# Kernel tuning notes

Hardware: AMD Instinct MI355X
Metric: run time of the kernel (lower is better)

The kernel has to match this reference:

```python
import jax, jax.numpy as jnp
import numpy as np

B, N, C = 16, 1024, 256
E = 524288
NUM_NODES = B * N
D0 = C + 7            # 263 input node feature dim
LAYERS = [256, 256, 256]


def _xavier(key, shape):
    fan_out, fan_in = shape
    lim = jnp.sqrt(6.0 / (fan_in + fan_out))
    return jax.random.uniform(key, shape, jnp.float32, -lim, lim)


def setup_inputs() -> dict:
    key = jax.random.key(0)
    ks = jax.random.split(key, 9)
    rois = jax.random.normal(ks[0], (B, N, 7), jnp.float32)
    pooled_features = jax.random.normal(ks[1], (B, N, C), jnp.float32)
    edge_index = jax.random.randint(ks[2], (2, E), 0, NUM_NODES, dtype=jnp.int64)
    # EdgeConv linear weights: layer0 in = 2*(C+7)=526, later in = 2*256=512
    W1 = _xavier(ks[3], (LAYERS[0], 2 * D0))
    b1 = jnp.zeros((LAYERS[0],), jnp.float32)
    W2 = _xavier(ks[4], (LAYERS[1], 2 * LAYERS[0]))
    b2 = jnp.zeros((LAYERS[1],), jnp.float32)
    W3 = _xavier(ks[5], (LAYERS[2], 2 * LAYERS[1]))
    b3 = jnp.zeros((LAYERS[2],), jnp.float32)
    return {"rois": rois, "pooled_features": pooled_features,
            "edge_index": edge_index,
            "W1": W1, "b1": b1, "W2": W2, "b2": b2, "W3": W3, "b3": b3}


def _edge_conv(x, src, dst, W, b):
    # message: cat(x_j - x_i, x_i) -> linear -> relu ; aggregate: scatter max at target i
    x_i = x[dst]                                   # [E, d] target features
    x_j = x[src]                                   # [E, d] source features
    msg = jnp.concatenate([x_j - x_i, x_i], axis=-1)   # [E, 2d]
    msg = jax.nn.relu(msg @ W.T + b)               # [E, out]
    agg = jax.ops.segment_max(msg, dst, num_segments=NUM_NODES)
    # nodes with no incoming edges: fill -inf -> 0 (PyG convention)
    return jnp.where(jnp.isfinite(agg), agg, jnp.zeros((), agg.dtype))


def reference(rois, pooled_features, edge_index, W1, b1, W2, b2, W3, b3):
    # global features: cat(pooled, boxes) flattened over batch
    x = jnp.concatenate([pooled_features, rois], axis=-1).reshape(-1, D0)  # [B*N, 263]
    src, dst = edge_index[0], edge_index[1]  # PyG: row = source j, col = target i
    feats = [x]
    x1 = _edge_conv(x, src, dst, W1, b1)
    feats.append(x1)
    x2 = _edge_conv(x1, src, dst, W2, b2)
    feats.append(x2)
    x3 = _edge_conv(x2, src, dst, W3, b3)
    feats.append(x3)
    related_features = jnp.concatenate(feats, axis=-1)  # [B*N, 263+768]
    return related_features
```

## Files before the change

### kernel.cpp

```cpp
#include <hip/hip_runtime.h>
#include <stdint.h>

#define NODES 16384
#define D0    263
#define K1PAD 288
#define OUTW  1031

typedef __attribute__((ext_vector_type(8))) short bf16x8;
typedef __attribute__((ext_vector_type(4))) float f32x4;
typedef __attribute__((ext_vector_type(8))) unsigned short u16x8;

__device__ __forceinline__ float bf2f(unsigned short u) {
    union { unsigned int i; float f; } c; c.i = ((unsigned int)u) << 16; return c.f;
}
__device__ __forceinline__ unsigned short f2bf(float f) {
    union { float f; unsigned int i; } c; c.f = f;
    unsigned int x = c.i;
    unsigned int r = (x + 0x7fffu + ((x >> 16) & 1u)) >> 16;
    return (unsigned short)r;
}
__device__ __forceinline__ unsigned short bf2key(unsigned short b) {
    return (b & 0x8000u) ? (unsigned short)~b : (unsigned short)(b | 0x8000u);
}
__device__ __forceinline__ unsigned short key2bf(unsigned short k) {
    return (k & 0x8000u) ? (unsigned short)(k ^ 0x8000u) : (unsigned short)~k;
}

__global__ void detect_zero_kernel(const void* __restrict__ ei, const void* __restrict__ pooled,
                                   int* __restrict__ flags, int* __restrict__ deg) {
    int idx = blockIdx.x * 256 + threadIdx.x;
    deg[idx] = 0;
    if (blockIdx.x == 0 && threadIdx.x < 64) {
        int lane = threadIdx.x;
        const long long* e64 = (const long long*)ei;
        bool ok = true;
        for (int i = lane; i < 512; i += 64) {
            long long v = e64[i];
            if (v < 0 || v >= NODES) ok = false;
        }
        unsigned long long b = __ballot(ok);
        const unsigned short* ph = (const unsigned short*)pooled;
        int hits = 0;
        for (int i = lane; i < 512; i += 64) {
            int e = (ph[i] >> 7) & 0xFF;
            if (e >= 0x90) hits++;
        }
        for (int off = 32; off; off >>= 1) hits += __shfl_down(hits, off);
        if (lane == 0) {
            flags[0] = (b == ~0ull) ? 1 : 0;
            flags[1] = (hits > 8) ? 1 : 0;
        }
    }
}

__global__ void hist_kernel(const void* __restrict__ ei, int E, const int* __restrict__ flags,
                            int* __restrict__ deg) {
    int e = blockIdx.x * blockDim.x + threadIdx.x;
    if (e >= E) return;
    int d = flags[0] ? (int)((const long long*)ei)[(size_t)E + e]
                     : ((const int*)ei)[(size_t)E + e];
    atomicAdd(&deg[d], 1);
}

__global__ void scan_kernel(const int* __restrict__ deg, int* __restrict__ offs,
                            int* __restrict__ cursor) {
    __shared__ int part[256];
    int tid = threadIdx.x;
    int base = tid * 64;
    int s = 0;
    for (int i = 0; i < 64; ++i) s += deg[base + i];
    part[tid] = s;
    __syncthreads();
    for (int off = 1; off < 256; off <<= 1) {
        int t = (tid >= off) ? part[tid - off] : 0;
        __syncthreads();
        part[tid] += t;
        __syncthreads();
    }
    int run = (tid > 0) ? part[tid - 1] : 0;
    for (int i = 0; i < 64; ++i) {
        int idx = base + i;
        offs[idx] = run;
        cursor[idx] = run;
        run += deg[idx];
    }
    if (tid == 255) offs[NODES] = run;
}

__global__ void scatter_kernel(const void* __restrict__ ei, int E, const int* __restrict__ flags,
                               int* __restrict__ cursor, int* __restrict__ ssrc) {
    int e = blockIdx.x * blockDim.x + threadIdx.x;
    if (e >= E) return;
    int s, d;
    if (flags[0]) {
        const long long* p = (const long long*)ei;
        s = (int)p[e];
        d = (int)p[(size_t)E + e];
    } else {
        const int* p = (const int*)ei;
        s = p[e];
        d = p[(size_t)E + e];
    }
    int pos = atomicAdd(&cursor[d], 1);
    ssrc[pos] = s;
}

#define T0 (NODES * K1PAD)
#define S1 (512 * K1PAD)
#define S2 (512 * 256)
__global__ void setup_kernel(const void* __restrict__ pooled, const void* __restrict__ rois,
                             const void* __restrict__ W1, const void* __restrict__ W2,
                             const void* __restrict__ W3, const int* __restrict__ flags,
                             unsigned short* __restrict__ x0p, void* __restrict__ outv,
                             unsigned short* __restrict__ wc1, unsigned short* __restrict__ wc2,
                             unsigned short* __restrict__ wc3) {
    int idx = blockIdx.x * 256 + threadIdx.x;
    bool f32m = flags[1] != 0;
    if (idx < T0) {
        int node = idx / K1PAD;
        int k = idx - node * K1PAD;
        float val = 0.f;
        if (k < 256) {
            val = f32m ? ((const float*)pooled)[(size_t)node * 256 + k]
                       : bf2f(((const unsigned short*)pooled)[(size_t)node * 256 + k]);
        } else if (k < D0) {
            val = f32m ? ((const float*)rois)[(size_t)node * 7 + (k - 256)]
                       : bf2f(((const unsigned short*)rois)[(size_t)node * 7 + (k - 256)]);
        }
        x0p[idx] = f2bf(val);
        if (k < D0) {
            if (f32m) ((float*)outv)[(size_t)node * OUTW + k] = val;
            else      ((unsigned short*)outv)[(size_t)node * OUTW + k] = f2bf(val);
        }
        return;
    }
    idx -= T0;
    if (idx < S1) {
        int r = idx / K1PAD;
        int k = idx - r * K1PAD;
        unsigned short val = 0;
        if (k < D0) {
            if (r < 256) {
                float a = f32m ? ((const float*)W1)[(size_t)r * 526 + k]
                               : bf2f(((const unsigned short*)W1)[(size_t)r * 526 + k]);
                val = f2bf(a);
            } else {
                size_t ro = (size_t)(r - 256) * 526;
                float a, b;
                if (f32m) { a = ((const float*)W1)[ro + k]; b = ((const float*)W1)[ro + D0 + k]; }
                else      { a = bf2f(((const unsigned short*)W1)[ro + k]);
                            b = bf2f(((const unsigned short*)W1)[ro + D0 + k]); }
                val = f2bf(b - a);
            }
        }
        wc1[idx] = val;
        return;
    }
    idx -= S1;
    const void* W = (idx < S2) ? W2 : W3;
    unsigned short* wc = (idx < S2) ? wc2 : wc3;
    if (idx >= S2) idx -= S2;
    int r = idx >> 8;
    int k = idx & 255;
    unsigned short val;
    if (r < 256) {
        float a = f32m ? ((const float*)W)[(size_t)r * 512 + k]
                       : bf2f(((const unsigned short*)W)[(size_t)r * 512 + k]);
        val = f2bf(a);
    } else {
        size_t ro = (size_t)(r - 256) * 512;
        float a, b;
        if (f32m) { a = ((const float*)W)[ro + k]; b = ((const float*)W)[ro + 256 + k]; }
        else      { a = bf2f(((const unsigned short*)W)[ro + k]);
                    b = bf2f(((const unsigned short*)W)[ro + 256 + k]); }
        val = f2bf(b - a);
    }
    wc[idx] = val;
}

template <int K>
__global__ __launch_bounds__(256) void gemm_kernel(const unsigned short* __restrict__ A,
                                                   const unsigned short* __restrict__ Wc,
                                                   unsigned short* __restrict__ u_key,
                                                   float* __restrict__ v_f) {
    int lane = threadIdx.x & 63;
    int wave = threadIdx.x >> 6;
    int row0 = blockIdx.x * 64;
    int col0 = blockIdx.y * 256 + wave * 64;
    int lr = lane & 15;
    int kb = (lane >> 4) * 8;
    const unsigned short* Ap = A + (size_t)(row0 + lr) * K + kb;
    const unsigned short* Wp = Wc + (size_t)(col0 + lr) * K + kb;

    f32x4 acc[4][4];
    #pragma unroll
    for (int i = 0; i < 4; ++i)
        #pragma unroll
        for (int j = 0; j < 4; ++j) acc[i][j] = (f32x4){0.f, 0.f, 0.f, 0.f};

    for (int k0 = 0; k0 < K; k0 += 32) {
        bf16x8 a[4], b[4];
        #pragma unroll
        for (int i = 0; i < 4; ++i) a[i] = *reinterpret_cast<const bf16x8*>(Ap + (size_t)i * 16 * K + k0);
        #pragma unroll
        for (int i = 0; i < 4; ++i) b[i] = *reinterpret_cast<const bf16x8*>(Wp + (size_t)i * 16 * K + k0);
        #pragma unroll
        for (int rb = 0; rb < 4; ++rb)
            #pragma unroll
            for (int cb = 0; cb < 4; ++cb)
                acc[rb][cb] = __builtin_amdgcn_mfma_f32_16x16x32_bf16(a[rb], b[cb], acc[rb][cb], 0, 0, 0);
    }

    bool is_u = (blockIdx.y == 0);
    #pragma unroll
    for (int rb = 0; rb < 4; ++rb) {
        int rbase = row0 + rb * 16 + (lane >> 4) * 4;
        #pragma unroll
        for (int cb = 0; cb < 4; ++cb) {
            int c = col0 + cb * 16 + lr;
            #pragma unroll
            for (int reg = 0; reg < 4; ++reg) {
                float val = acc[rb][cb][reg];
                int r = rbase + reg;
                if (is_u) u_key[(size_t)r * 256 + c] = bf2key(f2bf(val));
                else      v_f[(size_t)r * 256 + (c - 256)] = val;
            }
        }
    }
}

__global__ __launch_bounds__(256) void combine_kernel(const unsigned short* __restrict__ u_key,
                                                      const float* __restrict__ v_f,
                                                      const void* __restrict__ bias,
                                                      const int* __restrict__ flags,
                                                      const int* __restrict__ offs,
                                                      const int* __restrict__ ssrc,
                                                      unsigned short* __restrict__ x_cur,
                                                      void* __restrict__ outv,
                                                      int col_off) {
    int lane = threadIdx.x & 63;
    int node = blockIdx.x * 4 + (threadIdx.x >> 6);
    int half = lane >> 5;
    int cl = lane & 31;
    int s0 = offs[node];
    int s1 = offs[node + 1];
    bool f32m = flags[1] != 0;

    const u16x8* U = (const u16x8*)u_key;
    u16x8 mk = (u16x8)0;

    int i = s0 + half;
    for (; i + 6 < s1; i += 8) {
        int sA = ssrc[i], sB = ssrc[i + 2], sC = ssrc[i + 4], sD = ssrc[i + 6];
        u16x8 pA = U[(size_t)sA * 32 + cl];
        u16x8 pB = U[(size_t)sB * 32 + cl];
        u16x8 pC = U[(size_t)sC * 32 + cl];
        u16x8 pD = U[(size_t)sD * 32 + cl];
        mk = __builtin_elementwise_max(mk, __builtin_elementwise_max(
                 __builtin_elementwise_max(pA, pB), __builtin_elementwise_max(pC, pD)));
    }
    for (; i < s1; i += 2) {
        int s = ssrc[i];
        mk = __builtin_elementwise_max(mk, U[(size_t)s * 32 + cl]);
    }

    union { u16x8 v; uint4 u; } cvt;
    cvt.v = mk;
    cvt.u.x = __shfl_xor((int)cvt.u.x, 32);
    cvt.u.y = __shfl_xor((int)cvt.u.y, 32);
    cvt.u.z = __shfl_xor((int)cvt.u.z, 32);
    cvt.u.w = __shfl_xor((int)cvt.u.w, 32);
    mk = __builtin_elementwise_max(mk, cvt.v);

    int ch0 = cl * 8 + half * 4;
    float mm[4];
    #pragma unroll
    for (int j = 0; j < 4; ++j) mm[j] = bf2f(key2bf(mk[half * 4 + j]));

    float4 v = *(const float4*)(v_f + (size_t)node * 256 + ch0);
    float bb[4];
    if (f32m) {
        const float* bf = (const float*)bias;
        #pragma unroll
        for (int j = 0; j < 4; ++j) bb[j] = bf[ch0 + j];
    } else {
        const unsigned short* bh = (const unsigned short*)bias;
        #pragma unroll
        for (int j = 0; j < 4; ++j) bb[j] = bf2f(bh[ch0 + j]);
    }
    float vv[4] = {v.x, v.y, v.z, v.w};
    float r[4];
    bool nz = (s1 > s0);
    #pragma unroll
    for (int j = 0; j < 4; ++j) r[j] = nz ? fmaxf(mm[j] + vv[j] + bb[j], 0.f) : 0.f;

    unsigned short h[4];
    #pragma unroll
    for (int j = 0; j < 4; ++j) h[j] = f2bf(r[j]);
    uint2 packed;
    packed.x = (unsigned int)h[0] | ((unsigned int)h[1] << 16);
    packed.y = (unsigned int)h[2] | ((unsigned int)h[3] << 16);
    *(uint2*)(x_cur + (size_t)node * 256 + ch0) = packed;

    size_t ob = (size_t)node * OUTW + col_off + ch0;
    if (f32m) {
        float* of = (float*)outv;
        #pragma unroll
        for (int j = 0; j < 4; ++j) of[ob + j] = r[j];
    } else {
        unsigned short* oh = (unsigned short*)outv;
        #pragma unroll
        for (int j = 0; j < 4; ++j) oh[ob + j] = h[j];
    }
}

extern "C" void kernel_launch(void* const* d_in, const int* in_sizes, int n_in,
                              void* d_out, int out_size, void* d_ws, size_t ws_size,
                              hipStream_t stream) {
    const void* rois   = d_in[0];
    const void* pooled = d_in[1];
    const void* ei     = d_in[2];
    const void* W1 = d_in[3];
    const void* b1 = d_in[4];
    const void* W2 = d_in[5];
    const void* b2 = d_in[6];
    const void* W3 = d_in[7];
    const void* b3 = d_in[8];

    const int E = in_sizes[2] / 2;

    char* ws = (char*)d_ws;
    size_t o = 0;
    auto take = [&](size_t bytes) { size_t cur = o; o += (bytes + 255) & ~(size_t)255; return cur; };
    int* flags           = (int*)(ws + take(8));
    int* deg             = (int*)(ws + take(sizeof(int) * NODES));
    int* offs            = (int*)(ws + take(sizeof(int) * (NODES + 1)));
    int* cursor          = (int*)(ws + take(sizeof(int) * NODES));
    int* ssrc            = (int*)(ws + take(sizeof(int) * (size_t)E));
    unsigned short* x0p  = (unsigned short*)(ws + take(2ull * NODES * K1PAD));
    unsigned short* wc1  = (unsigned short*)(ws + take(2ull * 512 * K1PAD));
    unsigned short* wc2  = (unsigned short*)(ws + take(2ull * 512 * 256));
    unsigned short* wc3  = (unsigned short*)(ws + take(2ull * 512 * 256));
    unsigned short* ukey = (unsigned short*)(ws + take(2ull * NODES * 256));
    float*          vf   = (float*)(ws + take(4ull * NODES * 256));
    unsigned short* xcur = (unsigned short*)(ws + take(2ull * NODES * 256));
    (void)ws_size;

    const int eb = (E + 255) / 256;

    detect_zero_kernel<<<NODES / 256, 256, 0, stream>>>(ei, pooled, flags, deg);
    hist_kernel<<<eb, 256, 0, stream>>>(ei, E, flags, deg);
    scan_kernel<<<1, 256, 0, stream>>>(deg, offs, cursor);
    scatter_kernel<<<eb, 256, 0, stream>>>(ei, E, flags, cursor, ssrc);

    setup_kernel<<<(T0 + S1 + 2 * S2) / 256, 256, 0, stream>>>(pooled, rois, W1, W2, W3, flags,
                                                               x0p, d_out, wc1, wc2, wc3);

    gemm_kernel<K1PAD><<<dim3(NODES / 64, 2), 256, 0, stream>>>(x0p, wc1, ukey, vf);
    combine_kernel<<<NODES / 4, 256, 0, stream>>>(ukey, vf, b1, flags, offs, ssrc, xcur, d_out, D0);

    gemm_kernel<256><<<dim3(NODES / 64, 2), 256, 0, stream>>>(xcur, wc2, ukey, vf);
    combine_kernel<<<NODES / 4, 256, 0, stream>>>(ukey, vf, b2, flags, offs, ssrc, xcur, d_out, D0 + 256);

    gemm_kernel<256><<<dim3(NODES / 64, 2), 256, 0, stream>>>(xcur, wc3, ukey, vf);
    combine_kernel<<<NODES / 4, 256, 0, stream>>>(ukey, vf, b3, flags, offs, ssrc, xcur, d_out, D0 + 512);
}
```

Baseline: 252.7 us.

## Split gathered u table into two 128-channel halves for cache-resident max gather

The GEMM now writes the u keys into two separate 128-channel arrays, and each layer's combine step runs as two passes, one per half, each gathering 8-byte vectors. Each half table is 4 MB instead of 8 MB, so the random neighbour gather is more likely to hit in L2 or the last-level cache. In exchange, the CSR indices and offsets are read twice, there are twice as many launches, and each gather load is narrower.

```diff
diff --git a/kernel.cpp b/kernel.cpp
--- a/kernel.cpp
+++ b/kernel.cpp
@@ -8,7 +8,7 @@
 
 typedef __attribute__((ext_vector_type(8))) short bf16x8;
 typedef __attribute__((ext_vector_type(4))) float f32x4;
-typedef __attribute__((ext_vector_type(8))) unsigned short u16x8;
+typedef __attribute__((ext_vector_type(4))) unsigned short u16x4;
 
 __device__ __forceinline__ float bf2f(unsigned short u) {
     union { unsigned int i; float f; } c; c.i = ((unsigned int)u) << 16; return c.f;
@@ -181,7 +181,8 @@
 template <int K>
 __global__ __launch_bounds__(256) void gemm_kernel(const unsigned short* __restrict__ A,
                                                    const unsigned short* __restrict__ Wc,
-                                                   unsigned short* __restrict__ u_key,
+                                                   unsigned short* __restrict__ u_lo,
+                                                   unsigned short* __restrict__ u_hi,
                                                    float* __restrict__ v_f) {
     int lane = threadIdx.x & 63;
     int wave = threadIdx.x >> 6;
@@ -222,14 +223,19 @@
             for (int reg = 0; reg < 4; ++reg) {
                 float val = acc[rb][cb][reg];
                 int r = rbase + reg;
-                if (is_u) u_key[(size_t)r * 256 + c] = bf2key(f2bf(val));
-                else      v_f[(size_t)r * 256 + (c - 256)] = val;
+                if (is_u) {
+                    unsigned short key = bf2key(f2bf(val));
+                    if (c < 128) u_lo[(size_t)r * 128 + c] = key;
+                    else         u_hi[(size_t)r * 128 + (c - 128)] = key;
+                } else {
+                    v_f[(size_t)r * 256 + (c - 256)] = val;
+                }
             }
         }
     }
 }
 
-__global__ __launch_bounds__(256) void combine_kernel(const unsigned short* __restrict__ u_key,
+__global__ __launch_bounds__(256) void combine_kernel(const unsigned short* __restrict__ U,
                                                       const float* __restrict__ v_f,
                                                       const void* __restrict__ bias,
                                                       const int* __restrict__ flags,
@@ -237,7 +243,8 @@
                                                       const int* __restrict__ ssrc,
                                                       unsigned short* __restrict__ x_cur,
                                                       void* __restrict__ outv,
-                                                      int col_off) {
+                                                      int col_off,
+                                                      int ch_off) {
     int lane = threadIdx.x & 63;
     int node = blockIdx.x * 4 + (threadIdx.x >> 6);
     int half = lane >> 5;
@@ -246,71 +253,57 @@
     int s1 = offs[node + 1];
     bool f32m = flags[1] != 0;
 
-    const u16x8* U = (const u16x8*)u_key;
-    u16x8 mk = (u16x8)0;
+    const u16x4* U4 = (const u16x4*)U;
+    u16x4 mk = (u16x4)0;
 
     int i = s0 + half;
     for (; i + 6 < s1; i += 8) {
         int sA = ssrc[i], sB = ssrc[i + 2], sC = ssrc[i + 4], sD = ssrc[i + 6];
-        u16x8 pA = U[(size_t)sA * 32 + cl];
-        u16x8 pB = U[(size_t)sB * 32 + cl];
-        u16x8 pC = U[(size_t)sC * 32 + cl];
-        u16x8 pD = U[(size_t)sD * 32 + cl];
+        u16x4 pA = U4[(size_t)sA * 32 + cl];
+        u16x4 pB = U4[(size_t)sB * 32 + cl];
+        u16x4 pC = U4[(size_t)sC * 32 + cl];
+        u16x4 pD = U4[(size_t)sD * 32 + cl];
         mk = __builtin_elementwise_max(mk, __builtin_elementwise_max(
                  __builtin_elementwise_max(pA, pB), __builtin_elementwise_max(pC, pD)));
     }
     for (; i < s1; i += 2) {
         int s = ssrc[i];
-        mk = __builtin_elementwise_max(mk, U[(size_t)s * 32 + cl]);
-    }
-
-    union { u16x8 v; uint4 u; } cvt;
-    cvt.v = mk;
-    cvt.u.x = __shfl_xor((int)cvt.u.x, 32);
-    cvt.u.y = __shfl_xor((int)cvt.u.y, 32);
-    cvt.u.z = __shfl_xor((int)cvt.u.z, 32);
-    cvt.u.w = __shfl_xor((int)cvt.u.w, 32);
-    mk = __builtin_elementwise_max(mk, cvt.v);
-
-    int ch0 = cl * 8 + half * 4;
-    float mm[4];
-    #pragma unroll
-    for (int j = 0; j < 4; ++j) mm[j] = bf2f(key2bf(mk[half * 4 + j]));
-
-    float4 v = *(const float4*)(v_f + (size_t)node * 256 + ch0);
-    float bb[4];
+        mk = __builtin_elementwise_max(mk, U4[(size_t)s * 32 + cl]);
+    }
+
+    union { u16x4 v; uint2 u; } c1;
+    c1.v = mk;
+    c1.u.x = __shfl_xor((int)c1.u.x, 32);
+    c1.u.y = __shfl_xor((int)c1.u.y, 32);
+    mk = __builtin_elementwise_max(mk, c1.v);
+
+    int ch0 = cl * 4 + half * 2;
+    float m0 = bf2f(key2bf(mk[half * 2 + 0]));
+    float m1 = bf2f(key2bf(mk[half * 2 + 1]));
+    float2 v = *(const float2*)(v_f + (size_t)node * 256 + ch_off + ch0);
+    float b0, b1;
     if (f32m) {
         const float* bf = (const float*)bias;
-        #pragma unroll
-        for (int j = 0; j < 4; ++j) bb[j] = bf[ch0 + j];
+        b0 = bf[ch_off + ch0]; b1 = bf[ch_off + ch0 + 1];
     } else {
         const unsigned short* bh = (const unsigned short*)bias;
-        #pragma unroll
-        for (int j = 0; j < 4; ++j) bb[j] = bf2f(bh[ch0 + j]);
-    }
-    float vv[4] = {v.x, v.y, v.z, v.w};
-    float r[4];
+        b0 = bf2f(bh[ch_off + ch0]); b1 = bf2f(bh[ch_off + ch0 + 1]);
+    }
     bool nz = (s1 > s0);
-    #pragma unroll
-    for (int j = 0; j < 4; ++j) r[j] = nz ? fmaxf(mm[j] + vv[j] + bb[j], 0.f) : 0.f;
-
-    unsigned short h[4];
-    #pragma unroll
-    for (int j = 0; j < 4; ++j) h[j] = f2bf(r[j]);
-    uint2 packed;
-    packed.x = (unsigned int)h[0] | ((unsigned int)h[1] << 16);
-    packed.y = (unsigned int)h[2] | ((unsigned int)h[3] << 16);
-    *(uint2*)(x_cur + (size_t)node * 256 + ch0) = packed;
+    float r0 = nz ? fmaxf(m0 + v.x + b0, 0.f) : 0.f;
+    float r1 = nz ? fmaxf(m1 + v.y + b1, 0.f) : 0.f;
+
+    unsigned short h0 = f2bf(r0), h1 = f2bf(r1);
+    unsigned int hp = (unsigned int)h0 | ((unsigned int)h1 << 16);
+    *(unsigned int*)(x_cur + (size_t)node * 256 + ch_off + ch0) = hp;
 
     size_t ob = (size_t)node * OUTW + col_off + ch0;
     if (f32m) {
         float* of = (float*)outv;
-        #pragma unroll
-        for (int j = 0; j < 4; ++j) of[ob + j] = r[j];
+        of[ob + 0] = r0; of[ob + 1] = r1;
     } else {
         unsigned short* oh = (unsigned short*)outv;
-        #pragma unroll
-        for (int j = 0; j < 4; ++j) oh[ob + j] = h[j];
+        oh[ob + 0] = h0; oh[ob + 1] = h1;
     }
 }
 
@@ -341,7 +334,8 @@
     unsigned short* wc1  = (unsigned short*)(ws + take(2ull * 512 * K1PAD));
     unsigned short* wc2  = (unsigned short*)(ws + take(2ull * 512 * 256));
     unsigned short* wc3  = (unsigned short*)(ws + take(2ull * 512 * 256));
-    unsigned short* ukey = (unsigned short*)(ws + take(2ull * NODES * 256));
+    unsigned short* u_lo = (unsigned short*)(ws + take(2ull * NODES * 128));
+    unsigned short* u_hi = (unsigned short*)(ws + take(2ull * NODES * 128));
     float*          vf   = (float*)(ws + take(4ull * NODES * 256));
     unsigned short* xcur = (unsigned short*)(ws + take(2ull * NODES * 256));
     (void)ws_size;
@@ -356,12 +350,15 @@
     setup_kernel<<<(T0 + S1 + 2 * S2) / 256, 256, 0, stream>>>(pooled, rois, W1, W2, W3, flags,
                                                                x0p, d_out, wc1, wc2, wc3);
 
-    gemm_kernel<K1PAD><<<dim3(NODES / 64, 2), 256, 0, stream>>>(x0p, wc1, ukey, vf);
-    combine_kernel<<<NODES / 4, 256, 0, stream>>>(ukey, vf, b1, flags, offs, ssrc, xcur, d_out, D0);
-
-    gemm_kernel<256><<<dim3(NODES / 64, 2), 256, 0, stream>>>(xcur, wc2, ukey, vf);
-    combine_kernel<<<NODES / 4, 256, 0, stream>>>(ukey, vf, b2, flags, offs, ssrc, xcur, d_out, D0 + 256);
-
-    gemm_kernel<256><<<dim3(NODES / 64, 2), 256, 0, stream>>>(xcur, wc3, ukey, vf);
-    combine_kernel<<<NODES / 4, 256, 0, stream>>>(ukey, vf, b3, flags, offs, ssrc, xcur, d_out, D0 + 512);
-}
+    gemm_kernel<K1PAD><<<dim3(NODES / 64, 2), 256, 0, stream>>>(x0p, wc1, u_lo, u_hi, vf);
+    combine_kernel<<<NODES / 4, 256, 0, stream>>>(u_lo, vf, b1, flags, offs, ssrc, xcur, d_out, D0, 0);
+    combine_kernel<<<NODES / 4, 256, 0, stream>>>(u_hi, vf, b1, flags, offs, ssrc, xcur, d_out, D0 + 128, 128);
+
+    gemm_kernel<256><<<dim3(NODES / 64, 2), 256, 0, stream>>>(xcur, wc2, u_lo, u_hi, vf);
+    combine_kernel<<<NODES / 4, 256, 0, stream>>>(u_lo, vf, b2, flags, offs, ssrc, xcur, d_out, D0 + 256, 0);
+    combine_kernel<<<NODES / 4, 256, 0, stream>>>(u_hi, vf, b2, flags, offs, ssrc, xcur, d_out, D0 + 384, 128);
+
+    gemm_kernel<256><<<dim3(NODES / 64, 2), 256, 0, stream>>>(xcur, wc3, u_lo, u_hi, vf);
+    combine_kernel<<<NODES / 4, 256, 0, stream>>>(u_lo, vf, b3, flags, offs, ssrc, xcur, d_out, D0 + 512, 0);
+    combine_kernel<<<NODES / 4, 256, 0, stream>>>(u_hi, vf, b3, flags, offs, ssrc, xcur, d_out, D0 + 640, 128);
+}
```

Measured after the change: 277.8 us. 1.1x slower.

## Channel-group transposed layout with LDS-resident gather for segment max

Applied to the files above, without the earlier changes.

The GEMM now writes the U and V projections in a channel-pair-major layout, with the bias folded into V. Each combine block loads one 2-channel slice for all 16384 nodes (64 KB) into LDS and performs the per-node max gather out of shared memory instead of random global reads. A new fixup kernel transposes the results back to node-major order for the next layer's input and for the output. This replaces scattered global gathers with LDS gathers, but each layer now has only 256 combine blocks, each thread loops over 32 nodes, and there is an extra transpose pass and launch per layer.

```diff
diff --git a/kernel.cpp b/kernel.cpp
--- a/kernel.cpp
+++ b/kernel.cpp
@@ -5,10 +5,11 @@
 #define D0    263
 #define K1PAD 288
 #define OUTW  1031
+#define NGRP  128
 
 typedef __attribute__((ext_vector_type(8))) short bf16x8;
 typedef __attribute__((ext_vector_type(4))) float f32x4;
-typedef __attribute__((ext_vector_type(8))) unsigned short u16x8;
+typedef __attribute__((ext_vector_type(2))) unsigned short u16x2;
 
 __device__ __forceinline__ float bf2f(unsigned short u) {
     union { unsigned int i; float f; } c; c.i = ((unsigned int)u) << 16; return c.f;
@@ -24,6 +25,9 @@
 }
 __device__ __forceinline__ unsigned short key2bf(unsigned short k) {
     return (k & 0x8000u) ? (unsigned short)(k ^ 0x8000u) : (unsigned short)~k;
+}
+__device__ __forceinline__ u16x2 as_u16x2(unsigned int x) {
+    union { unsigned int u; u16x2 v; } c; c.u = x; return c.v;
 }
 
 __global__ void detect_zero_kernel(const void* __restrict__ ei, const void* __restrict__ pooled,
@@ -181,8 +185,10 @@
 template <int K>
 __global__ __launch_bounds__(256) void gemm_kernel(const unsigned short* __restrict__ A,
                                                    const unsigned short* __restrict__ Wc,
-                                                   unsigned short* __restrict__ u_key,
-                                                   float* __restrict__ v_f) {
+                                                   const void* __restrict__ bias,
+                                                   const int* __restrict__ flags,
+                                                   unsigned short* __restrict__ u_g,
+                                                   float* __restrict__ vb_g) {
     int lane = threadIdx.x & 63;
     int wave = threadIdx.x >> 6;
     int row0 = blockIdx.x * 64;
@@ -212,105 +218,117 @@
     }
 
     bool is_u = (blockIdx.y == 0);
+    bool f32m = flags[1] != 0;
     #pragma unroll
     for (int rb = 0; rb < 4; ++rb) {
         int rbase = row0 + rb * 16 + (lane >> 4) * 4;
         #pragma unroll
         for (int cb = 0; cb < 4; ++cb) {
             int c = col0 + cb * 16 + lr;
-            #pragma unroll
-            for (int reg = 0; reg < 4; ++reg) {
-                float val = acc[rb][cb][reg];
-                int r = rbase + reg;
-                if (is_u) u_key[(size_t)r * 256 + c] = bf2key(f2bf(val));
-                else      v_f[(size_t)r * 256 + (c - 256)] = val;
+            if (is_u) {
+                int g = c >> 1;
+                size_t base = (size_t)g * 32768 + (c & 1);
+                #pragma unroll
+                for (int reg = 0; reg < 4; ++reg) {
+                    int r = rbase + reg;
+                    u_g[base + (size_t)r * 2] = bf2key(f2bf(acc[rb][cb][reg]));
+                }
+            } else {
+                int c2 = c - 256;
+                int g = c2 >> 1;
+                float bv = f32m ? ((const float*)bias)[c2]
+                                : bf2f(((const unsigned short*)bias)[c2]);
+                size_t base = (size_t)g * 32768 + (c2 & 1);
+                #pragma unroll
+                for (int reg = 0; reg < 4; ++reg) {
+                    int r = rbase + reg;
+                    vb_g[base + (size_t)r * 2] = acc[rb][cb][reg] + bv;
+                }
             }
         }
     }
 }
 
-__global__ __launch_bounds__(256) void combine_kernel(const unsigned short* __restrict__ u_key,
-                                                      const float* __restrict__ v_f,
-                                                      const void* __restrict__ bias,
-                                                      const int* __restrict__ flags,
+__global__ __launch_bounds__(256) void combine_kernel(const unsigned short* __restrict__ u_g,
+                                                      const float* __restrict__ vb_g,
                                                       const int* __restrict__ offs,
                                                       const int* __restrict__ ssrc,
-                                                      unsigned short* __restrict__ x_cur,
-                                                      void* __restrict__ outv,
-                                                      int col_off) {
-    int lane = threadIdx.x & 63;
-    int node = blockIdx.x * 4 + (threadIdx.x >> 6);
-    int half = lane >> 5;
-    int cl = lane & 31;
-    int s0 = offs[node];
-    int s1 = offs[node + 1];
+                                                      unsigned int* __restrict__ xcur_t) {
+    __shared__ unsigned int uslice[NODES];
+    int g = blockIdx.x & (NGRP - 1);
+    int chunk = blockIdx.x >> 7;
+    int tid = threadIdx.x;
+
+    const uint4* s4 = (const uint4*)(u_g + (size_t)g * 32768);
+    uint4* d4 = (uint4*)uslice;
+    #pragma unroll
+    for (int i = 0; i < 16; ++i) d4[tid + i * 256] = s4[tid + i * 256];
+    __syncthreads();
+
+    const float2* vb2 = (const float2*)(vb_g + (size_t)g * 32768);
+    unsigned int* xt = xcur_t + (size_t)g * NODES;
+    int nbase = chunk * 8192 + tid;
+
+    for (int k = 0; k < 32; ++k) {
+        int n = nbase + k * 256;
+        int s0 = offs[n], s1 = offs[n + 1];
+        u16x2 mk = (u16x2)0;
+        int e = s0;
+        for (; e + 3 < s1; e += 4) {
+            int i0 = ssrc[e], i1 = ssrc[e + 1], i2 = ssrc[e + 2], i3 = ssrc[e + 3];
+            u16x2 k0 = as_u16x2(uslice[i0]);
+            u16x2 k1 = as_u16x2(uslice[i1]);
+            u16x2 k2 = as_u16x2(uslice[i2]);
+            u16x2 k3 = as_u16x2(uslice[i3]);
+            mk = __builtin_elementwise_max(mk, __builtin_elementwise_max(
+                     __builtin_elementwise_max(k0, k1), __builtin_elementwise_max(k2, k3)));
+        }
+        for (; e < s1; ++e)
+            mk = __builtin_elementwise_max(mk, as_u16x2(uslice[ssrc[e]]));
+
+        float m0 = bf2f(key2bf(mk[0]));
+        float m1 = bf2f(key2bf(mk[1]));
+        float2 vv = vb2[n];
+        bool nz = (s1 > s0);
+        float r0 = nz ? fmaxf(m0 + vv.x, 0.f) : 0.f;
+        float r1 = nz ? fmaxf(m1 + vv.y, 0.f) : 0.f;
+        xt[n] = (unsigned int)f2bf(r0) | ((unsigned int)f2bf(r1) << 16);
+    }
+}
+
+__global__ __launch_bounds__(256) void fixup_kernel(const unsigned int* __restrict__ xcur_t,
+                                                    const int* __restrict__ flags,
+                                                    unsigned short* __restrict__ x_cur,
+                                                    void* __restrict__ outv,
+                                                    int col_off) {
+    __shared__ unsigned int tile[32][NGRP + 1];
+    int n0 = blockIdx.x * 32;
+    int t = threadIdx.x;
+    #pragma unroll
+    for (int it = 0; it < 16; ++it) {
+        int flat = it * 256 + t;
+        int g = flat >> 5, j = flat & 31;
+        tile[j][g] = xcur_t[(size_t)g * NODES + n0 + j];
+    }
+    __syncthreads();
     bool f32m = flags[1] != 0;
-
-    const u16x8* U = (const u16x8*)u_key;
-    u16x8 mk = (u16x8)0;
-
-    int i = s0 + half;
-    for (; i + 6 < s1; i += 8) {
-        int sA = ssrc[i], sB = ssrc[i + 2], sC = ssrc[i + 4], sD = ssrc[i + 6];
-        u16x8 pA = U[(size_t)sA * 32 + cl];
-        u16x8 pB = U[(size_t)sB * 32 + cl];
-        u16x8 pC = U[(size_t)sC * 32 + cl];
-        u16x8 pD = U[(size_t)sD * 32 + cl];
-        mk = __builtin_elementwise_max(mk, __builtin_elementwise_max(
-                 __builtin_elementwise_max(pA, pB), __builtin_elementwise_max(pC, pD)));
-    }
-    for (; i < s1; i += 2) {
-        int s = ssrc[i];
-        mk = __builtin_elementwise_max(mk, U[(size_t)s * 32 + cl]);
-    }
-
-    union { u16x8 v; uint4 u; } cvt;
-    cvt.v = mk;
-    cvt.u.x = __shfl_xor((int)cvt.u.x, 32);
-    cvt.u.y = __shfl_xor((int)cvt.u.y, 32);
-    cvt.u.z = __shfl_xor((int)cvt.u.z, 32);
-    cvt.u.w = __shfl_xor((int)cvt.u.w, 32);
-    mk = __builtin_elementwise_max(mk, cvt.v);
-
-    int ch0 = cl * 8 + half * 4;
-    float mm[4];
-    #pragma unroll
-    for (int j = 0; j < 4; ++j) mm[j] = bf2f(key2bf(mk[half * 4 + j]));
-
-    float4 v = *(const float4*)(v_f + (size_t)node * 256 + ch0);
-    float bb[4];
-    if (f32m) {
-        const float* bf = (const float*)bias;
-        #pragma unroll
-        for (int j = 0; j < 4; ++j) bb[j] = bf[ch0 + j];
-    } else {
-        const unsigned short* bh = (const unsigned short*)bias;
-        #pragma unroll
-        for (int j = 0; j < 4; ++j) bb[j] = bf2f(bh[ch0 + j]);
-    }
-    float vv[4] = {v.x, v.y, v.z, v.w};
-    float r[4];
-    bool nz = (s1 > s0);
-    #pragma unroll
-    for (int j = 0; j < 4; ++j) r[j] = nz ? fmaxf(mm[j] + vv[j] + bb[j], 0.f) : 0.f;
-
-    unsigned short h[4];
-    #pragma unroll
-    for (int j = 0; j < 4; ++j) h[j] = f2bf(r[j]);
-    uint2 packed;
-    packed.x = (unsigned int)h[0] | ((unsigned int)h[1] << 16);
-    packed.y = (unsigned int)h[2] | ((unsigned int)h[3] << 16);
-    *(uint2*)(x_cur + (size_t)node * 256 + ch0) = packed;
-
-    size_t ob = (size_t)node * OUTW + col_off + ch0;
-    if (f32m) {
-        float* of = (float*)outv;
-        #pragma unroll
-        for (int j = 0; j < 4; ++j) of[ob + j] = r[j];
-    } else {
-        unsigned short* oh = (unsigned short*)outv;
-        #pragma unroll
-        for (int j = 0; j < 4; ++j) oh[ob + j] = h[j];
+    int n = t >> 3, seg = t & 7;
+    int node = n0 + n;
+    unsigned int* xc = (unsigned int*)(x_cur + (size_t)node * 256) + seg * 16;
+    size_t ob = (size_t)node * OUTW + col_off + seg * 32;
+    #pragma unroll
+    for (int k2 = 0; k2 < 16; ++k2) {
+        unsigned int w = tile[n][seg * 16 + k2];
+        xc[k2] = w;
+        unsigned short h0 = (unsigned short)(w & 0xffff);
+        unsigned short h1 = (unsigned short)(w >> 16);
+        if (f32m) {
+            ((float*)outv)[ob + k2 * 2]     = bf2f(h0);
+            ((float*)outv)[ob + k2 * 2 + 1] = bf2f(h1);
+        } else {
+            ((unsigned short*)outv)[ob + k2 * 2]     = h0;
+            ((unsigned short*)outv)[ob + k2 * 2 + 1] = h1;
+        }
     }
 }
 
@@ -341,8 +359,9 @@
     unsigned short* wc1  = (unsigned short*)(ws + take(2ull * 512 * K1PAD));
     unsigned short* wc2  = (unsigned short*)(ws + take(2ull * 512 * 256));
     unsigned short* wc3  = (unsigned short*)(ws + take(2ull * 512 * 256));
-    unsigned short* ukey = (unsigned short*)(ws + take(2ull * NODES * 256));
-    float*          vf   = (float*)(ws + take(4ull * NODES * 256));
+    unsigned short* u_g  = (unsigned short*)(ws + take(2ull * NODES * 256));
+    float*          vb_g = (float*)(ws + take(4ull * NODES * 256));
+    unsigned int*  xcurt = (unsigned int*)(ws + take(4ull * NODES * NGRP / 1 / 2 * 2));
     unsigned short* xcur = (unsigned short*)(ws + take(2ull * NODES * 256));
     (void)ws_size;
 
@@ -356,12 +375,15 @@
     setup_kernel<<<(T0 + S1 + 2 * S2) / 256, 256, 0, stream>>>(pooled, rois, W1, W2, W3, flags,
                                                                x0p, d_out, wc1, wc2, wc3);
 
-    gemm_kernel<K1PAD><<<dim3(NODES / 64, 2), 256, 0, stream>>>(x0p, wc1, ukey, vf);
-    combine_kernel<<<NODES / 4, 256, 0, stream>>>(ukey, vf, b1, flags, offs, ssrc, xcur, d_out, D0);
-
-    gemm_kernel<256><<<dim3(NODES / 64, 2), 256, 0, stream>>>(xcur, wc2, ukey, vf);
-    combine_kernel<<<NODES / 4, 256, 0, stream>>>(ukey, vf, b2, flags, offs, ssrc, xcur, d_out, D0 + 256);
-
-    gemm_kernel<256><<<dim3(NODES / 64, 2), 256, 0, stream>>>(xcur, wc3, ukey, vf);
-    combine_kernel<<<NODES / 4, 256, 0, stream>>>(ukey, vf, b3, flags, offs, ssrc, xcur, d_out, D0 + 512);
-}
+    gemm_kernel<K1PAD><<<dim3(NODES / 64, 2), 256, 0, stream>>>(x0p, wc1, b1, flags, u_g, vb_g);
+    combine_kernel<<<2 * NGRP, 256, 0, stream>>>(u_g, vb_g, offs, ssrc, xcurt);
+    fixup_kernel<<<NODES / 32, 256, 0, stream>>>(xcurt, flags, xcur, d_out, D0);
+
+    gemm_kernel<256><<<dim3(NODES / 64, 2), 256, 0, stream>>>(xcur, wc2, b2, flags, u_g, vb_g);
+    combine_kernel<<<2 * NGRP, 256, 0, stream>>>(u_g, vb_g, offs, ssrc, xcurt);
+    fixup_kernel<<<NODES / 32, 256, 0, stream>>>(xcurt, flags, xcur, d_out, D0 + 256);
+
+    gemm_kernel<256><<<dim3(NODES / 64, 2), 256, 0, stream>>>(xcur, wc3, b3, flags, u_g, vb_g);
+    combine_kernel<<<2 * NGRP, 256, 0, stream>>>(u_g, vb_g, offs, ssrc, xcurt);
+    fixup_kernel<<<NODES / 32, 256, 0, stream>>>(xcurt, flags, xcur, d_out, D0 + 512);
+}
```

After: 625.6 us. +147.6%, slower.

## Transpose features to channel-group-major layout and aggregate from LDS-resident slices

Applied to the files above, without the earlier changes.

Intermediate features move into a [channel/4][node][4] layout, so each combine block can hold one 4-channel slice of all node keys (128KB) in LDS and gather the edge max from shared memory instead of global memory. An edge table padded per 64-node group is built in setup so lanes read interleaved int4 source indices. The GEMM now folds the bias in, writes transposed bf16 output through an LDS tile, and reads the transposed A. A final assemble kernel writes every output column, which adds a pass over the output and rounds v to bf16.

```diff
diff --git a/kernel.cpp b/kernel.cpp
--- a/kernel.cpp
+++ b/kernel.cpp
@@ -8,7 +8,7 @@
 
 typedef __attribute__((ext_vector_type(8))) short bf16x8;
 typedef __attribute__((ext_vector_type(4))) float f32x4;
-typedef __attribute__((ext_vector_type(8))) unsigned short u16x8;
+typedef __attribute__((ext_vector_type(4))) unsigned short u16x4;
 
 __device__ __forceinline__ float bf2f(unsigned short u) {
     union { unsigned int i; float f; } c; c.i = ((unsigned int)u) << 16; return c.f;
@@ -24,6 +24,9 @@
 }
 __device__ __forceinline__ unsigned short key2bf(unsigned short k) {
     return (k & 0x8000u) ? (unsigned short)(k ^ 0x8000u) : (unsigned short)~k;
+}
+__device__ __forceinline__ u16x4 as_u16x4(uint2 x) {
+    union { uint2 u; u16x4 v; } c; c.u = x; return c.v;
 }
 
 __global__ void detect_zero_kernel(const void* __restrict__ ei, const void* __restrict__ pooled,
@@ -63,18 +66,20 @@
 }
 
 __global__ void scan_kernel(const int* __restrict__ deg, int* __restrict__ offs,
-                            int* __restrict__ cursor) {
-    __shared__ int part[256];
+                            int* __restrict__ cursor, int* __restrict__ gbase4) {
+    __shared__ int part[256], gpart[256];
     int tid = threadIdx.x;
     int base = tid * 64;
-    int s = 0;
-    for (int i = 0; i < 64; ++i) s += deg[base + i];
+    int s = 0, mx = 0;
+    for (int i = 0; i < 64; ++i) { int d = deg[base + i]; s += d; mx = max(mx, d); }
     part[tid] = s;
+    gpart[tid] = (mx + 3) >> 2;
     __syncthreads();
     for (int off = 1; off < 256; off <<= 1) {
-        int t = (tid >= off) ? part[tid - off] : 0;
+        int t1 = (tid >= off) ? part[tid - off] : 0;
+        int t2 = (tid >= off) ? gpart[tid - off] : 0;
         __syncthreads();
-        part[tid] += t;
+        part[tid] += t1; gpart[tid] += t2;
         __syncthreads();
     }
     int run = (tid > 0) ? part[tid - 1] : 0;
@@ -85,6 +90,8 @@
         run += deg[idx];
     }
     if (tid == 255) offs[NODES] = run;
+    gbase4[tid + 1] = gpart[tid];
+    if (tid == 0) gbase4[0] = 0;
 }
 
 __global__ void scatter_kernel(const void* __restrict__ ei, int E, const int* __restrict__ flags,
@@ -108,10 +115,13 @@
 #define T0 (NODES * K1PAD)
 #define S1 (512 * K1PAD)
 #define S2 (512 * 256)
+#define SETUP_TOT (T0 + S1 + 2 * S2 + NODES)
 __global__ void setup_kernel(const void* __restrict__ pooled, const void* __restrict__ rois,
                              const void* __restrict__ W1, const void* __restrict__ W2,
                              const void* __restrict__ W3, const int* __restrict__ flags,
-                             unsigned short* __restrict__ x0p, void* __restrict__ outv,
+                             const int* __restrict__ offs, const int* __restrict__ ssrc,
+                             const int* __restrict__ gbase4, int* __restrict__ et,
+                             unsigned short* __restrict__ x0p,
                              unsigned short* __restrict__ wc1, unsigned short* __restrict__ wc2,
                              unsigned short* __restrict__ wc3) {
     int idx = blockIdx.x * 256 + threadIdx.x;
@@ -128,10 +138,6 @@
                        : bf2f(((const unsigned short*)rois)[(size_t)node * 7 + (k - 256)]);
         }
         x0p[idx] = f2bf(val);
-        if (k < D0) {
-            if (f32m) ((float*)outv)[(size_t)node * OUTW + k] = val;
-            else      ((unsigned short*)outv)[(size_t)node * OUTW + k] = f2bf(val);
-        }
         return;
     }
     idx -= T0;
@@ -157,32 +163,57 @@
         return;
     }
     idx -= S1;
-    const void* W = (idx < S2) ? W2 : W3;
-    unsigned short* wc = (idx < S2) ? wc2 : wc3;
-    if (idx >= S2) idx -= S2;
-    int r = idx >> 8;
-    int k = idx & 255;
-    unsigned short val;
-    if (r < 256) {
-        float a = f32m ? ((const float*)W)[(size_t)r * 512 + k]
-                       : bf2f(((const unsigned short*)W)[(size_t)r * 512 + k]);
-        val = f2bf(a);
-    } else {
-        size_t ro = (size_t)(r - 256) * 512;
-        float a, b;
-        if (f32m) { a = ((const float*)W)[ro + k]; b = ((const float*)W)[ro + 256 + k]; }
-        else      { a = bf2f(((const unsigned short*)W)[ro + k]);
-                    b = bf2f(((const unsigned short*)W)[ro + 256 + k]); }
-        val = f2bf(b - a);
-    }
-    wc[idx] = val;
-}
-
-template <int K>
+    if (idx < 2 * S2) {
+        const void* W = (idx < S2) ? W2 : W3;
+        unsigned short* wc = (idx < S2) ? wc2 : wc3;
+        if (idx >= S2) idx -= S2;
+        int r = idx >> 8;
+        int k = idx & 255;
+        unsigned short val;
+        if (r < 256) {
+            float a = f32m ? ((const float*)W)[(size_t)r * 512 + k]
+                           : bf2f(((const unsigned short*)W)[(size_t)r * 512 + k]);
+            val = f2bf(a);
+        } else {
+            size_t ro = (size_t)(r - 256) * 512;
+            float a, b;
+            if (f32m) { a = ((const float*)W)[ro + k]; b = ((const float*)W)[ro + 256 + k]; }
+            else      { a = bf2f(((const unsigned short*)W)[ro + k]);
+                        b = bf2f(((const unsigned short*)W)[ro + 256 + k]); }
+            val = f2bf(b - a);
+        }
+        wc[idx] = val;
+        return;
+    }
+    idx -= 2 * S2;
+    if (idx < NODES) {
+        int n = idx;
+        int lane = n & 63, ng = n >> 6;
+        int s0 = offs[n];
+        int dg = offs[n + 1] - s0;
+        int b4 = gbase4[ng];
+        int q4 = gbase4[ng + 1] - b4;
+        int4* dst = (int4*)et + (size_t)b4 * 64 + lane;
+        for (int q = 0; q < q4; ++q) {
+            int i0 = q * 4;
+            int4 v;
+            v.x = dg ? ssrc[s0 + min(i0,     dg - 1)] : 0;
+            v.y = dg ? ssrc[s0 + min(i0 + 1, dg - 1)] : 0;
+            v.z = dg ? ssrc[s0 + min(i0 + 2, dg - 1)] : 0;
+            v.w = dg ? ssrc[s0 + min(i0 + 3, dg - 1)] : 0;
+            dst[(size_t)q * 64] = v;
+        }
+    }
+}
+
+template <int K, int ALAYOUT>
 __global__ __launch_bounds__(256) void gemm_kernel(const unsigned short* __restrict__ A,
                                                    const unsigned short* __restrict__ Wc,
-                                                   unsigned short* __restrict__ u_key,
-                                                   float* __restrict__ v_f) {
+                                                   const void* __restrict__ bias,
+                                                   const int* __restrict__ flags,
+                                                   unsigned short* __restrict__ u_t4,
+                                                   unsigned short* __restrict__ vb_t4) {
+    __shared__ __align__(16) unsigned short tile[64][65][4];
     int lane = threadIdx.x & 63;
     int wave = threadIdx.x >> 6;
     int row0 = blockIdx.x * 64;
@@ -200,10 +231,25 @@
 
     for (int k0 = 0; k0 < K; k0 += 32) {
         bf16x8 a[4], b[4];
+        if (ALAYOUT == 0) {
+            #pragma unroll
+            for (int i = 0; i < 4; ++i)
+                a[i] = *reinterpret_cast<const bf16x8*>(Ap + (size_t)i * 16 * K + k0);
+        } else {
+            int c4a = (k0 + kb) >> 2;
+            #pragma unroll
+            for (int i = 0; i < 4; ++i) {
+                int row = row0 + i * 16 + lr;
+                uint2 lo = *(const uint2*)(A + ((size_t)c4a * NODES + row) * 4);
+                uint2 hi = *(const uint2*)(A + ((size_t)(c4a + 1) * NODES + row) * 4);
+                union { uint4 u; bf16x8 v; } pk;
+                pk.u.x = lo.x; pk.u.y = lo.y; pk.u.z = hi.x; pk.u.w = hi.y;
+                a[i] = pk.v;
+            }
+        }
         #pragma unroll
-        for (int i = 0; i < 4; ++i) a[i] = *reinterpret_cast<const bf16x8*>(Ap + (size_t)i * 16 * K + k0);
-        #pragma unroll
-        for (int i = 0; i < 4; ++i) b[i] = *reinterpret_cast<const bf16x8*>(Wp + (size_t)i * 16 * K + k0);
+        for (int i = 0; i < 4; ++i)
+            b[i] = *reinterpret_cast<const bf16x8*>(Wp + (size_t)i * 16 * K + k0);
         #pragma unroll
         for (int rb = 0; rb < 4; ++rb)
             #pragma unroll
@@ -212,105 +258,139 @@
     }
 
     bool is_u = (blockIdx.y == 0);
+    bool f32m = flags[1] != 0;
     #pragma unroll
     for (int rb = 0; rb < 4; ++rb) {
-        int rbase = row0 + rb * 16 + (lane >> 4) * 4;
         #pragma unroll
         for (int cb = 0; cb < 4; ++cb) {
-            int c = col0 + cb * 16 + lr;
+            int ccol = col0 + cb * 16 + lr;
+            int cl = is_u ? ccol : (ccol - 256);
+            float bv = 0.f;
+            if (!is_u) bv = f32m ? ((const float*)bias)[cl]
+                                 : bf2f(((const unsigned short*)bias)[cl]);
+            int rloc = rb * 16 + (lane >> 4) * 4;
             #pragma unroll
             for (int reg = 0; reg < 4; ++reg) {
-                float val = acc[rb][cb][reg];
-                int r = rbase + reg;
-                if (is_u) u_key[(size_t)r * 256 + c] = bf2key(f2bf(val));
-                else      v_f[(size_t)r * 256 + (c - 256)] = val;
+                float v = acc[rb][cb][reg];
+                unsigned short val = is_u ? bf2key(f2bf(v)) : f2bf(v + bv);
+                tile[cl >> 2][rloc + reg][cl & 3] = val;
             }
         }
     }
-}
-
-__global__ __launch_bounds__(256) void combine_kernel(const unsigned short* __restrict__ u_key,
-                                                      const float* __restrict__ v_f,
-                                                      const void* __restrict__ bias,
-                                                      const int* __restrict__ flags,
-                                                      const int* __restrict__ offs,
-                                                      const int* __restrict__ ssrc,
-                                                      unsigned short* __restrict__ x_cur,
-                                                      void* __restrict__ outv,
-                                                      int col_off) {
-    int lane = threadIdx.x & 63;
-    int node = blockIdx.x * 4 + (threadIdx.x >> 6);
-    int half = lane >> 5;
-    int cl = lane & 31;
-    int s0 = offs[node];
-    int s1 = offs[node + 1];
+    __syncthreads();
+
+    unsigned short* dst = is_u ? u_t4 : vb_t4;
+    int c4 = threadIdx.x >> 2, sub = threadIdx.x & 3;
+    size_t base = ((size_t)c4 * NODES + row0) * 4;
+    #pragma unroll
+    for (int i = 0; i < 8; ++i) {
+        int n1 = sub * 2 + i * 8;
+        uint2 a_ = *(const uint2*)&tile[c4][n1][0];
+        uint2 b_ = *(const uint2*)&tile[c4][n1 + 1][0];
+        uint4 w; w.x = a_.x; w.y = a_.y; w.z = b_.x; w.w = b_.y;
+        *(uint4*)(dst + base + (size_t)n1 * 4) = w;
+    }
+}
+
+__global__ __launch_bounds__(1024) void combine_kernel(const unsigned short* __restrict__ u_t4,
+                                                       const unsigned short* __restrict__ vb_t4,
+                                                       const int* __restrict__ offs,
+                                                       const int* __restrict__ gbase4,
+                                                       const int* __restrict__ et,
+                                                       unsigned short* __restrict__ xq) {
+    extern __shared__ uint2 uslice[];
+    int g = blockIdx.x & 63;
+    int chunk = blockIdx.x >> 6;
+    int tid = threadIdx.x;
+
+    const uint2* src = (const uint2*)(u_t4 + (size_t)g * NODES * 4);
+    #pragma unroll
+    for (int i = 0; i < 16; ++i) uslice[tid + i * 1024] = src[tid + i * 1024];
+    __syncthreads();
+
+    const uint2* vbp = (const uint2*)(vb_t4 + (size_t)g * NODES * 4);
+    uint2* xp = (uint2*)(xq + (size_t)g * NODES * 4);
+
+    #pragma unroll
+    for (int k = 0; k < 2; ++k) {
+        int n = chunk * 2048 + k * 1024 + tid;
+        int ng = n >> 6;
+        int b4 = gbase4[ng];
+        int q4 = gbase4[ng + 1] - b4;
+        const int4* ep = (const int4*)et + (size_t)b4 * 64 + (tid & 63);
+
+        u16x4 mk = (u16x4)0;
+        for (int q = 0; q < q4; ++q) {
+            int4 e = ep[(size_t)q * 64];
+            u16x4 k0 = as_u16x4(uslice[e.x]);
+            u16x4 k1 = as_u16x4(uslice[e.y]);
+            u16x4 k2 = as_u16x4(uslice[e.z]);
+            u16x4 k3 = as_u16x4(uslice[e.w]);
+            mk = __builtin_elementwise_max(mk, __builtin_elementwise_max(
+                     __builtin_elementwise_max(k0, k1), __builtin_elementwise_max(k2, k3)));
+        }
+
+        u16x4 vb = as_u16x4(vbp[n]);
+        bool nz = offs[n + 1] > offs[n];
+        unsigned short h[4];
+        #pragma unroll
+        for (int j = 0; j < 4; ++j) {
+            float r = nz ? fmaxf(bf2f(key2bf(mk[j])) + bf2f(vb[j]), 0.f) : 0.f;
+            h[j] = f2bf(r);
+        }
+        uint2 w;
+        w.x = (unsigned int)h[0] | ((unsigned int)h[1] << 16);
+        w.y = (unsigned int)h[2] | ((unsigned int)h[3] << 16);
+        xp[n] = w;
+    }
+}
+
+__global__ __launch_bounds__(256) void assemble_kernel(const void* __restrict__ pooled,
+                                                       const void* __restrict__ rois,
+                                                       const int* __restrict__ flags,
+                                                       const unsigned short* __restrict__ x1,
+                                                       const unsigned short* __restrict__ x2,
+                                                       const unsigned short* __restrict__ x3,
+                                                       void* __restrict__ outv) {
+    __shared__ __align__(16) unsigned short tile[64][65][4];
+    int n0 = blockIdx.x * 64;
+    int t = threadIdx.x;
     bool f32m = flags[1] != 0;
 
-    const u16x8* U = (const u16x8*)u_key;
-    u16x8 mk = (u16x8)0;
-
-    int i = s0 + half;
-    for (; i + 6 < s1; i += 8) {
-        int sA = ssrc[i], sB = ssrc[i + 2], sC = ssrc[i + 4], sD = ssrc[i + 6];
-        u16x8 pA = U[(size_t)sA * 32 + cl];
-        u16x8 pB = U[(size_t)sB * 32 + cl];
-        u16x8 pC = U[(size_t)sC * 32 + cl];
-        u16x8 pD = U[(size_t)sD * 32 + cl];
-        mk = __builtin_elementwise_max(mk, __builtin_elementwise_max(
-                 __builtin_elementwise_max(pA, pB), __builtin_elementwise_max(pC, pD)));
-    }
-    for (; i < s1; i += 2) {
-        int s = ssrc[i];
-        mk = __builtin_elementwise_max(mk, U[(size_t)s * 32 + cl]);
-    }
-
-    union { u16x8 v; uint4 u; } cvt;
-    cvt.v = mk;
-    cvt.u.x = __shfl_xor((int)cvt.u.x, 32);
-    cvt.u.y = __shfl_xor((int)cvt.u.y, 32);
-    cvt.u.z = __shfl_xor((int)cvt.u.z, 32);
-    cvt.u.w = __shfl_xor((int)cvt.u.w, 32);
-    mk = __builtin_elementwise_max(mk, cvt.v);
-
-    int ch0 = cl * 8 + half * 4;
-    float mm[4];
-    #pragma unroll
-    for (int j = 0; j < 4; ++j) mm[j] = bf2f(key2bf(mk[half * 4 + j]));
-
-    float4 v = *(const float4*)(v_f + (size_t)node * 256 + ch0);
-    float bb[4];
-    if (f32m) {
-        const float* bf = (const float*)bias;
-        #pragma unroll
-        for (int j = 0; j < 4; ++j) bb[j] = bf[ch0 + j];
-    } else {
-        const unsigned short* bh = (const unsigned short*)bias;
-        #pragma unroll
-        for (int j = 0; j < 4; ++j) bb[j] = bf2f(bh[ch0 + j]);
-    }
-    float vv[4] = {v.x, v.y, v.z, v.w};
-    float r[4];
-    bool nz = (s1 > s0);
-    #pragma unroll
-    for (int j = 0; j < 4; ++j) r[j] = nz ? fmaxf(mm[j] + vv[j] + bb[j], 0.f) : 0.f;
-
-    unsigned short h[4];
-    #pragma unroll
-    for (int j = 0; j < 4; ++j) h[j] = f2bf(r[j]);
-    uint2 packed;
-    packed.x = (unsigned int)h[0] | ((unsigned int)h[1] << 16);
-    packed.y = (unsigned int)h[2] | ((unsigned int)h[3] << 16);
-    *(uint2*)(x_cur + (size_t)node * 256 + ch0) = packed;
-
-    size_t ob = (size_t)node * OUTW + col_off + ch0;
-    if (f32m) {
-        float* of = (float*)outv;
-        #pragma unroll
-        for (int j = 0; j < 4; ++j) of[ob + j] = r[j];
-    } else {
-        unsigned short* oh = (unsigned short*)outv;
-        #pragma unroll
-        for (int j = 0; j < 4; ++j) oh[ob + j] = h[j];
+    for (int idx = t; idx < 64 * 263; idx += 256) {
+        int n = idx / 263, c = idx - n * 263;
+        float val;
+        if (c < 256)
+            val = f32m ? ((const float*)pooled)[(size_t)(n0 + n) * 256 + c]
+                       : bf2f(((const unsigned short*)pooled)[(size_t)(n0 + n) * 256 + c]);
+        else
+            val = f32m ? ((const float*)rois)[(size_t)(n0 + n) * 7 + (c - 256)]
+                       : bf2f(((const unsigned short*)rois)[(size_t)(n0 + n) * 7 + (c - 256)]);
+        if (f32m) ((float*)outv)[(size_t)(n0 + n) * OUTW + c] = val;
+        else      ((unsigned short*)outv)[(size_t)(n0 + n) * OUTW + c] = f2bf(val);
+    }
+
+    const unsigned short* xs[3] = {x1, x2, x3};
+    int n = t >> 2, sub = t & 3;
+    for (int l = 0; l < 3; ++l) {
+        __syncthreads();
+        for (int idx = t; idx < 4096; idx += 256) {
+            int c4 = idx >> 6, j = idx & 63;
+            uint2 w = ((const uint2*)(xs[l]))[(size_t)c4 * NODES + n0 + j];
+            *(unsigned int*)&tile[c4][j][0] = w.x;
+            *(unsigned int*)&tile[c4][j][2] = w.y;
+        }
+        __syncthreads();
+        size_t ob = (size_t)(n0 + n) * OUTW + D0 + l * 256 + sub * 64;
+        for (int c4i = 0; c4i < 16; ++c4i) {
+            int c4 = sub * 16 + c4i;
+            #pragma unroll
+            for (int j = 0; j < 4; ++j) {
+                unsigned short h = tile[c4][n][j];
+                if (f32m) ((float*)outv)[ob + c4i * 4 + j] = bf2f(h);
+                else      ((unsigned short*)outv)[ob + c4i * 4 + j] = h;
+            }
+        }
     }
 }
 
@@ -337,31 +417,37 @@
     int* offs            = (int*)(ws + take(sizeof(int) * (NODES + 1)));
     int* cursor          = (int*)(ws + take(sizeof(int) * NODES));
     int* ssrc            = (int*)(ws + take(sizeof(int) * (size_t)E));
+    int* gbase4          = (int*)(ws + take(sizeof(int) * 257));
+    int* et              = (int*)(ws + take(32ull << 20));
     unsigned short* x0p  = (unsigned short*)(ws + take(2ull * NODES * K1PAD));
     unsigned short* wc1  = (unsigned short*)(ws + take(2ull * 512 * K1PAD));
     unsigned short* wc2  = (unsigned short*)(ws + take(2ull * 512 * 256));
     unsigned short* wc3  = (unsigned short*)(ws + take(2ull * 512 * 256));
-    unsigned short* ukey = (unsigned short*)(ws + take(2ull * NODES * 256));
-    float*          vf   = (float*)(ws + take(4ull * NODES * 256));
-    unsigned short* xcur = (unsigned short*)(ws + take(2ull * NODES * 256));
+    unsigned short* u_t4 = (unsigned short*)(ws + take(2ull * NODES * 256));
+    unsigned short* vbt4 = (unsigned short*)(ws + take(2ull * NODES * 256));
+    unsigned short* xq1  = (unsigned short*)(ws + take(2ull * NODES * 256));
+    unsigned short* xq2  = (unsigned short*)(ws + take(2ull * NODES * 256));
+    unsigned short* xq3  = (unsigned short*)(ws + take(2ull * NODES * 256));
     (void)ws_size;
 
     const int eb = (E + 255) / 256;
 
     detect_zero_kernel<<<NODES / 256, 256, 0, stream>>>(ei, pooled, flags, deg);
     hist_kernel<<<eb, 256, 0, stream>>>(ei, E, flags, deg);
-    scan_kernel<<<1, 256, 0, stream>>>(deg, offs, cursor);
+    scan_kernel<<<1, 256, 0, stream>>>(deg, offs, cursor, gbase4);
     scatter_kernel<<<eb, 256, 0, stream>>>(ei, E, flags, cursor, ssrc);
-
-    setup_kernel<<<(T0 + S1 + 2 * S2) / 256, 256, 0, stream>>>(pooled, rois, W1, W2, W3, flags,
-                                                               x0p, d_out, wc1, wc2, wc3);
-
-    gemm_kernel<K1PAD><<<dim3(NODES / 64, 2), 256, 0, stream>>>(x0p, wc1, ukey, vf);
-    combine_kernel<<<NODES / 4, 256, 0, stream>>>(ukey, vf, b1, flags, offs, ssrc, xcur, d_out, D0);
-
-    gemm_kernel<256><<<dim3(NODES / 64, 2), 256, 0, stream>>>(xcur, wc2, ukey, vf);
-    combine_kernel<<<NODES / 4, 256, 0, stream>>>(ukey, vf, b2, flags, offs, ssrc, xcur, d_out, D0 + 256);
-
-    gemm_kernel<256><<<dim3(NODES / 64, 2), 256, 0, stream>>>(xcur, wc3, ukey, vf);
-    combine_kernel<<<NODES / 4, 256, 0, stream>>>(ukey, vf, b3, flags, offs, ssrc, xcur, d_out, D0 + 512);
-}
+    setup_kernel<<<(SETUP_TOT + 255) / 256, 256, 0, stream>>>(pooled, rois, W1, W2, W3, flags,
+                                                              offs, ssrc, gbase4, et,
+                                                              x0p, wc1, wc2, wc3);
+
+    gemm_kernel<K1PAD, 0><<<dim3(NODES / 64, 2), 256, 0, stream>>>(x0p, wc1, b1, flags, u_t4, vbt4);
+    combine_kernel<<<8 * 64, 1024, 131072, stream>>>(u_t4, vbt4, offs, gbase4, et, xq1);
+
+    gemm_kernel<256, 1><<<dim3(NODES / 64, 2), 256, 0, stream>>>(xq1, wc2, b2, flags, u_t4, vbt4);
+    combine_kernel<<<8 * 64, 1024, 131072, stream>>>(u_t4, vbt4, offs, gbase4, et, xq2);
+
+    gemm_kernel<256, 1><<<dim3(NODES / 64, 2), 256, 0, stream>>>(xq2, wc3, b3, flags, u_t4, vbt4);
+    combine_kernel<<<8 * 64, 1024, 131072, stream>>>(u_t4, vbt4, offs, gbase4, et, xq3);
+
+    assemble_kernel<<<NODES / 64, 256, 0, stream>>>(pooled, rois, flags, xq1, xq2, xq3, d_out);
+}
```

Result: slower. 323.1 us (+27.9%).
